# Kernel optimization log

Hardware: AMD Instinct MI355X
Metric: run time of the kernel (lower is better)

The kernel has to match this reference:

```python
import jax, jax.numpy as jnp
import numpy as np

NZ = 128
N_GEN = 8
BATCH = 2048
SLOPE = 0.2


def _convt(x, w, b, stride, pad):
    # PyTorch ConvTranspose2d(weight [Cin,Cout,kH,kW], stride, padding p)
    # == conv with lhs_dilation=stride, padding=k-1-p, spatially-flipped
    # kernel with in/out channels swapped.
    k = jnp.flip(w, axis=(2, 3)).transpose(2, 3, 0, 1)  # [kH,kW,Cin,Cout]
    y = jax.lax.conv_general_dilated(
        x, k, window_strides=(1, 1), padding=[(pad, pad), (pad, pad)],
        lhs_dilation=(stride, stride),
        dimension_numbers=('NCHW', 'HWIO', 'NCHW'))
    return y + b[None, :, None, None]


def setup_inputs() -> dict:
    key = jax.random.key(0)
    ks = jax.random.split(key, 12)
    s = 0.05
    return {
        'z': jax.random.normal(ks[0], (BATCH, NZ), jnp.float32),
        'g_idx': jax.random.randint(ks[1], (BATCH,), 0, N_GEN),
        'W1': jax.random.normal(ks[2], (N_GEN, NZ, 256), jnp.float32) * s,
        'b1': jax.random.normal(ks[3], (N_GEN, 256), jnp.float32) * s,
        'W2': jax.random.normal(ks[4], (N_GEN, 256, 1568), jnp.float32) * s,
        'b2': jax.random.normal(ks[5], (N_GEN, 1568), jnp.float32) * s,
        'cw1': jax.random.normal(ks[6], (N_GEN, 32, 16, 4, 4), jnp.float32) * s,
        'cb1': jax.random.normal(ks[7], (N_GEN, 16), jnp.float32) * s,
        'cw2': jax.random.normal(ks[8], (N_GEN, 16, 8, 4, 4), jnp.float32) * s,
        'cb2': jax.random.normal(ks[9], (N_GEN, 8), jnp.float32) * s,
        'cw3': jax.random.normal(ks[10], (N_GEN, 8, 1, 3, 3), jnp.float32) * s,
        'cb3': jax.random.normal(ks[11], (N_GEN, 1), jnp.float32) * s,
    }


def _single_gen(params, z):
    W1, b1, W2, b2, cw1, cb1, cw2, cb2, cw3, cb3 = params
    lrelu = lambda x: jax.nn.leaky_relu(x, SLOPE)
    h = lrelu(z @ W1 + b1)                 # [B,256]
    h = lrelu(h @ W2 + b2)                 # [B,1568]
    h = h.reshape(-1, 32, 7, 7)
    h = lrelu(_convt(h, cw1, cb1, 2, 2))   # [B,16,14,14]
    h = lrelu(_convt(h, cw2, cb2, 2, 2))   # [B,8,28,28]
    return jnp.tanh(_convt(h, cw3, cb3, 1, 1))  # [B,1,28,28]


def reference(z, g_idx, W1, b1, W2, b2, cw1, cb1, cw2, cb2, cw3, cb3):
    params = (W1, b1, W2, b2, cw1, cb1, cw2, cb2, cw3, cb3)
    # Compute every generator on the full batch (faithful to the torch loop),
    # vmapped over the generator axis: images [G,B,1,28,28].
    images = jax.vmap(_single_gen, in_axes=((0,) * 10, None))(params, z)
    # Per-sample gather: keep generator g_idx[b] for each sample b.
    return images[g_idx, jnp.arange(z.shape[0])]
```

## Files before the change

### kernel.cpp

```cpp
#include <hip/hip_runtime.h>
#include <cstdint>
#include <cstddef>

#define BATCH 2048
#define NZ 128
#define NGEN 8
#define GRPS 32
#define MAXG 72
#define NCT 13
#define H2_ELEMS 1792
#define WS_H1_OFF 16384
#define WS_H2_OFF (16384 + MAXG * 8192 * 4)
#define WS_W2T_OFF (WS_H2_OFF + BATCH * H2_ELEMS * 2)
#define W2T_GSTRIDE (1568 * 256)
#define NB_W2T (NGEN * 49)
#define NB_PREP (NB_W2T + MAXG * 4)
#define WS_WPK1_OFF (WS_W2T_OFF + NGEN * W2T_GSTRIDE * 2)
#define WS_WPK2_OFF (WS_WPK1_OFF + NGEN * 4096 * 4)
#define WS_WPK3_OFF (WS_WPK2_OFF + NGEN * 1024 * 4)
#define PS 168

typedef unsigned int u32;
typedef unsigned short u16;
typedef unsigned long long u64;
typedef _Float16 f16x8 __attribute__((ext_vector_type(8)));
typedef _Float16 f16x4 __attribute__((ext_vector_type(4)));
typedef _Float16 f16x2 __attribute__((ext_vector_type(2)));
typedef float f32x4 __attribute__((ext_vector_type(4)));

__device__ __forceinline__ float lrelu(float x) { return fmaxf(x, 0.2f * x); }
__device__ __forceinline__ u16 f16b(float f) {
    _Float16 h = (_Float16)f;
    return __builtin_bit_cast(u16, h);
}
__device__ __forceinline__ u32 pk2(float a, float b) {
    f16x2 v; v[0] = (_Float16)a; v[1] = (_Float16)b;
    return __builtin_bit_cast(u32, v);
}
__device__ __forceinline__ float dot2(u32 a, u32 b, float c) {
#if __has_builtin(__builtin_amdgcn_fdot2)
    return __builtin_amdgcn_fdot2(__builtin_bit_cast(f16x2, a),
                                  __builtin_bit_cast(f16x2, b), c, false);
#else
    float d;
    asm("v_dot2_f32_f16 %0, %1, %2, %3" : "=v"(d) : "v"(a), "v"(b), "v"(c));
    return d;
#endif
}
__device__ __forceinline__ float fast_tanh(float x) {
    x = fminf(fmaxf(x, -9.f), 9.f);
    const float e = __expf(2.f * x);
    return (e - 1.f) / (e + 1.f);
}
__device__ __forceinline__ int h2off(int n) {
    const int ci = n / 49, rm = n % 49;
    return ci * 56 + (rm / 7) * 8 + (rm % 7);
}

__global__ __launch_bounds__(256) void prep_kernel(
    const float* __restrict__ z, const int* __restrict__ g_idx,
    const float* __restrict__ W1, const float* __restrict__ b1,
    const float* __restrict__ W2, int* __restrict__ wsi,
    float* __restrict__ h1g, _Float16* __restrict__ W2T,
    const float* __restrict__ cw1, const float* __restrict__ cw2,
    const float* __restrict__ cw3,
    u32* __restrict__ wpk1, u32* __restrict__ wpk2, u32* __restrict__ wpk3)
{
    __shared__ __align__(16) char pmem[16896];

    const int tid = threadIdx.x;
    const int bx = blockIdx.x;

    if (bx < NB_W2T) {
        _Float16 (*t)[264] = (_Float16 (*)[264])pmem;
        const int g = bx / 49;
        const int n0 = (bx % 49) * 32;
        const float* src = W2 + (size_t)g * 256 * 1568;
        const int nl = tid & 31, kh = tid >> 5;
        #pragma unroll 8
        for (int p = 0; p < 32; ++p) {
            const int k = p * 8 + kh;
            t[nl][k] = (_Float16)src[(size_t)k * 1568 + n0 + nl];
        }
        __syncthreads();
        _Float16* dst = W2T + (size_t)g * W2T_GSTRIDE + (size_t)n0 * 256;
        #pragma unroll
        for (int ii = 0; ii < 4; ++ii) {
            const int i = tid + 256 * ii;
            const int n = i >> 5, kc = i & 31;
            *(uint4*)(dst + (size_t)n * 256 + kc * 8) = *(const uint4*)&t[n][kc * 8];
        }
        return;
    }

    if (bx >= NB_PREP && bx < NB_PREP + NGEN) {
        const int g = bx - NB_PREP;
        const float* c1p = cw1 + g * 8192;
        u32* o1 = wpk1 + g * 4096;
        for (int i = tid; i < 4096; i += 256) {
            const int cip = i >> 8, a = (i >> 6) & 3, co = (i >> 2) & 15, c = i & 3;
            const float* s = c1p + cip * 512 + co * 16 + a * 4 + c;
            o1[i] = pk2(s[0], s[256]);
        }
        const float* c2p = cw2 + g * 2048;
        u32* o2 = wpk2 + g * 1024;
        for (int i = tid; i < 1024; i += 256) {
            const int cip = i >> 7, a = (i >> 5) & 3, co = (i >> 2) & 7, c = i & 3;
            const float* s = c2p + cip * 256 + co * 16 + a * 4 + c;
            o2[i] = pk2(s[0], s[128]);
        }
        if (tid < 36) {
            const int cip = tid / 9, r = tid % 9;
            const float* s = cw3 + g * 72 + cip * 18 + r;
            wpk3[g * 36 + tid] = pk2(s[0], s[9]);
        }
        return;
    }

    u16* rank       = (u16*)pmem;
    int (*wcnt)[NGEN]  = (int (*)[NGEN])(pmem + 4096);
    int (*wboff)[NGEN] = (int (*)[NGEN])(pmem + 4224);
    int* pbase      = (int*)(pmem + 4352);
    const int w = tid >> 6, lane = tid & 63;
    if (tid < 4 * NGEN) wcnt[tid >> 3][tid & 7] = 0;
    __syncthreads();
    const u64 lt = ((u64)1 << lane) - 1;
    #pragma unroll
    for (int r = 0; r < 8; ++r) {
        const int b = r * 256 + tid;
        const int gg = g_idx[b];
        u64 m[NGEN];
        #pragma unroll
        for (int k = 0; k < NGEN; ++k) m[k] = __ballot(gg == k);
        rank[b] = (u16)((int)__popcll(m[gg] & lt) + wcnt[w][gg]);
        if (lane < NGEN) wcnt[w][lane] += (int)__popcll(m[lane]);
    }
    __syncthreads();
    if (tid == 0) {
        int acc = 0;
        for (int g = 0; g < NGEN; ++g) {
            pbase[g] = acc;
            const int tot = wcnt[0][g] + wcnt[1][g] + wcnt[2][g] + wcnt[3][g];
            acc += ((tot + GRPS - 1) / GRPS) * GRPS;
        }
        pbase[NGEN] = acc;
    }
    __syncthreads();
    if (tid < 32) {
        const int ww = tid >> 3, g = tid & 7;
        int off = pbase[g];
        for (int w2 = 0; w2 < ww; ++w2) off += wcnt[w2][g];
        wboff[ww][g] = off;
    }
    __syncthreads();

    if (bx >= NB_PREP + NGEN) {
        if (tid == 0) wsi[0] = pbase[NGEN];
        for (int i = tid; i < MAXG * GRPS; i += 256) wsi[16 + i] = -1;
        __syncthreads();
        #pragma unroll
        for (int r = 0; r < 8; ++r) {
            const int b = r * 256 + tid;
            const int gg = g_idx[b];
            wsi[16 + wboff[w][gg] + (int)rank[b]] = b;
        }
        return;
    }

    const int bx2 = bx - NB_W2T;
    const int grp = bx2 >> 2;
    const int s0 = (bx2 & 3) * 8;
    if (grp * GRPS >= pbase[NGEN]) return;

    int gsel = 0;
    #pragma unroll
    for (int g = 1; g < NGEN; ++g) if (grp * GRPS >= pbase[g]) gsel = g;

    int* sb = (int*)(pmem + 4400);
    float (*zst)[12] = (float (*)[12])(pmem + 4608);
    if (tid < 8) sb[tid] = -1;
    __syncthreads();
    const int base = grp * GRPS + s0;
    #pragma unroll
    for (int r = 0; r < 8; ++r) {
        const int b = r * 256 + tid;
        const int gg = g_idx[b];
        const int rel = wboff[w][gg] + (int)rank[b] - base;
        if ((unsigned)rel < 8u) sb[rel] = b;
    }
    __syncthreads();

    const float* W1g = W1 + gsel * (NZ * 256);
    const float* b1g = b1 + gsel * 256;

    {
        const int s = tid >> 5, f = tid & 31;
        float4 v = make_float4(0.f, 0.f, 0.f, 0.f);
        if (sb[s] >= 0) v = *(const float4*)(z + (size_t)sb[s] * NZ + 4 * f);
        zst[4 * f + 0][s] = v.x; zst[4 * f + 1][s] = v.y;
        zst[4 * f + 2][s] = v.z; zst[4 * f + 3][s] = v.w;
    }
    __syncthreads();

    const int c = tid;
    float acc[8];
    #pragma unroll
    for (int s = 0; s < 8; ++s) acc[s] = 0.f;
    const float* wp = W1g + c;
    #pragma unroll 4
    for (int k = 0; k < NZ; ++k) {
        const float wv = wp[k * 256];
        float av[8];
        *(float4*)&av[0] = *(const float4*)&zst[k][0];
        *(float4*)&av[4] = *(const float4*)&zst[k][4];
        #pragma unroll
        for (int s = 0; s < 8; ++s) acc[s] += av[s] * wv;
    }
    const float bv = b1g[c];
    float* hp = h1g + (size_t)grp * 8192 + (size_t)s0 * 256 + c;
    #pragma unroll
    for (int s = 0; s < 8; ++s) hp[s * 256] = lrelu(acc[s] + bv);
}

__global__ __launch_bounds__(256) void fc2_kernel(
    const int* __restrict__ g_idx,
    const _Float16* __restrict__ W2T, const float* __restrict__ b2,
    const int* __restrict__ wsi, const float* __restrict__ h1g,
    u16* __restrict__ h2g)
{
    __shared__ __align__(16) char afsm[16384];
    _Float16* afrag = (_Float16*)afsm;
    __shared__ int sb[GRPS];
    __shared__ int sG;

    const int tid = threadIdx.x;
    const int grp = blockIdx.x / NCT;
    const int tile = blockIdx.x % NCT;
    if (grp * GRPS >= wsi[0]) return;

    if (tid == 0) sG = g_idx[wsi[16 + grp * GRPS]];
    if (tid < GRPS) sb[tid] = wsi[16 + grp * GRPS + tid];
    __syncthreads();
    const _Float16* W2Tg = W2T + (size_t)sG * W2T_GSTRIDE;
    const float* b2g = b2 + sG * 1568;

    {
        const float4* h1p4 = (const float4*)(h1g + (size_t)grp * 8192);
        #pragma unroll
        for (int i = 0; i < 8; ++i) {
            const int u = tid + 256 * i;
            const int j4 = u & 1;
            const int ln = (u >> 1) & 63;
            const int kq = (u >> 7) & 7;
            const int mt = (u >> 10) & 1;
            const int s = mt * 16 + (ln & 15);
            const float4 v = h1p4[s * 64 + kq * 8 + ((ln >> 4) << 1) + j4];
            f16x4 hi;
            hi[0] = (_Float16)v.x; hi[1] = (_Float16)v.y;
            hi[2] = (_Float16)v.z; hi[3] = (_Float16)v.w;
            const int bh = ((mt * 8 + kq) * 64 + ln) * 8 + 4 * j4;
            *(f16x4*)&afrag[bh] = hi;
        }
    }
    __syncthreads();

    const int wave = tid >> 6;
    const int lane = tid & 63;
    const int q = lane >> 4;
    const int nl = lane & 15;
    const int nb0 = tile * 128 + 2 * wave * 16;
    const int nb1 = nb0 + 16;
    const bool act0 = nb0 < 1568, act1 = nb1 < 1568;

    f32x4 accA0 = {0.f, 0.f, 0.f, 0.f}, accB0 = accA0;
    f32x4 accA1 = accA0, accB1 = accA0;
    if (act0) {
        const _Float16* bp = W2Tg + (size_t)(nb0 + nl) * 256 + q * 8;
        #pragma unroll
        for (int kq = 0; kq < 8; ++kq) {
            const f16x8 b = *(const f16x8*)(bp + kq * 32);
            const f16x8 a0 = *(const f16x8*)&afrag[((0 * 8 + kq) * 64 + lane) * 8];
            const f16x8 a1 = *(const f16x8*)&afrag[((1 * 8 + kq) * 64 + lane) * 8];
            accA0 = __builtin_amdgcn_mfma_f32_16x16x32_f16(a0, b, accA0, 0, 0, 0);
            accB0 = __builtin_amdgcn_mfma_f32_16x16x32_f16(a1, b, accB0, 0, 0, 0);
        }
    }
    if (act1) {
        const _Float16* bp = W2Tg + (size_t)(nb1 + nl) * 256 + q * 8;
        #pragma unroll
        for (int kq = 0; kq < 8; ++kq) {
            const f16x8 b = *(const f16x8*)(bp + kq * 32);
            const f16x8 a0 = *(const f16x8*)&afrag[((0 * 8 + kq) * 64 + lane) * 8];
            const f16x8 a1 = *(const f16x8*)&afrag[((1 * 8 + kq) * 64 + lane) * 8];
            accA1 = __builtin_amdgcn_mfma_f32_16x16x32_f16(a0, b, accA1, 0, 0, 0);
            accB1 = __builtin_amdgcn_mfma_f32_16x16x32_f16(a1, b, accB1, 0, 0, 0);
        }
    }
    __syncthreads();

    u16* pst = (u16*)afsm;
    const int nstart = tile * 128;
    const int nend = (nstart + 128 < 1568) ? nstart + 128 : 1568;
    const int offLo = h2off(nstart), offHi = h2off(nend - 1);
    const int lo8 = offLo & ~7;

    if (act0) {
        const int n = nb0 + nl;
        const float bias = b2g[n];
        u16* pp = pst + (h2off(n) - lo8);
        #pragma unroll
        for (int reg = 0; reg < 4; ++reg) {
            pp[(q * 4 + reg) * PS]        = f16b(lrelu(accA0[reg] + bias));
            pp[(16 + q * 4 + reg) * PS]   = f16b(lrelu(accB0[reg] + bias));
        }
    }
    if (act1) {
        const int n = nb1 + nl;
        const float bias = b2g[n];
        u16* pp = pst + (h2off(n) - lo8);
        #pragma unroll
        for (int reg = 0; reg < 4; ++reg) {
            pp[(q * 4 + reg) * PS]        = f16b(lrelu(accA1[reg] + bias));
            pp[(16 + q * 4 + reg) * PS]   = f16b(lrelu(accB1[reg] + bias));
        }
    }
    __syncthreads();

    {
        const int s = tid >> 3, p = tid & 7;
        const int bb = sb[s];
        if (bb >= 0) {
            u16* row = h2g + (size_t)bb * H2_ELEMS;
            const u16* ps = pst + s * PS - lo8;
            const int c0 = (offLo + 7) & ~7;
            const int c1 = (offHi + 1) & ~7;
            for (int o = offLo + p; o < c0 && o <= offHi; o += 8) row[o] = ps[o];
            const int t0 = (c1 > offLo) ? c1 : offLo;
            for (int o = t0 + p; o <= offHi; o += 8) row[o] = ps[o];
            for (int c = c0 + p * 8; c + 8 <= c1; c += 64)
                *(uint4*)(row + c) = *(const uint4*)(ps + c);
        }
    }
}

template <int H>
__device__ __forceinline__ void conv2p_half(
    const u32 (*c1s)[14][20], u16* dst,
    const u32* __restrict__ w2g, const float bv, const int co, const int y)
{
    float acc[14];
    #pragma unroll
    for (int xx = 0; xx < 14; ++xx) acc[xx] = bv;
    const int a0 = (y + 1) & 1;
    for (int aa = 0; aa < 2; ++aa) {
        const int a = a0 + 2 * aa;
        const int iy = (y + 1 - a) >> 1;
        if ((unsigned)iy < 14u) {
            #pragma unroll 4
            for (int cip = 0; cip < 8; ++cip) {
                u32 rr[10];
                if (H == 0) {
                    *(uint4*)&rr[0] = *(const uint4*)&c1s[cip][iy][0];
                    *(uint4*)&rr[4] = *(const uint4*)&c1s[cip][iy][4];
                } else {
                    *(uint4*)&rr[0] = *(const uint4*)&c1s[cip][iy][4];
                    *(uint4*)&rr[4] = *(const uint4*)&c1s[cip][iy][8];
                    *(uint2*)&rr[8] = *(const uint2*)&c1s[cip][iy][12];
                }
                const uint4 wq = *(const uint4*)(w2g + ((cip * 4 + a) * 8 + co) * 4);
                const u32 wv[4] = {wq.x, wq.y, wq.z, wq.w};
                #pragma unroll
                for (int xx = 0; xx < 14; ++xx) {
                    const int x = 14 * H + xx;
                    const int c0v = (x + 1) & 1;
                    const int ix0 = (x + 1 - c0v) >> 1;
                    const int li = ix0 - 4 * H;
                    if (ix0 < 14) acc[xx] = dot2(rr[li],     wv[c0v],     acc[xx]);
                    if (ix0 >= 1) acc[xx] = dot2(rr[li - 1], wv[c0v + 2], acc[xx]);
                }
            }
        }
    }
    #pragma unroll
    for (int xx = 0; xx < 14; ++xx) dst[2 * (14 * H + xx)] = f16b(lrelu(acc[xx]));
}

__global__ __launch_bounds__(256, 6) void conv_kernel(
    const int* __restrict__ g_idx, const int* __restrict__ wsi,
    const u32* __restrict__ wpk1, const float* __restrict__ cb1,
    const u32* __restrict__ wpk2, const float* __restrict__ cb2,
    const u32* __restrict__ wpk3, const float* __restrict__ cb3,
    const u16* __restrict__ h2g, float* __restrict__ out)
{
    __shared__ __align__(16) char smem[8960 + 14784];
    u32 (*c1s)[14][20] = (u32 (*)[14][20])smem;
    u32 (*h2s)[7][8]   = (u32 (*)[7][8])(smem + 8960);
    u32 (*c2s)[28][33] = (u32 (*)[28][33])(smem + 8960);
    __shared__ u32 w3s[36];

    const int tid = threadIdx.x;
    const int b = wsi[16 + blockIdx.x];
    if (b < 0) return;
    const int g = g_idx[b];
    const u32* w1g = wpk1 + g * 4096;
    const u32* w2g = wpk2 + g * 1024;
    const float* cb1g = cb1 + g * 16;
    const float* cb2g = cb2 + g * 8;
    const float  cb3v = cb3[g];

    if (tid < 224) {
        const uint4 qv = ((const uint4*)(h2g + (size_t)b * H2_ELEMS))[tid];
        const int ci = tid / 7, yq = tid % 7;
        u16* dst = (u16*)&h2s[ci >> 1][yq][0] + (ci & 1);
        const u32 w[4] = {qv.x, qv.y, qv.z, qv.w};
        #pragma unroll
        for (int j = 0; j < 4; ++j) {
            dst[4 * j]     = (u16)(w[j] & 0xffffu);
            dst[4 * j + 2] = (u16)(w[j] >> 16);
        }
    }
    if (tid < 36) w3s[tid] = wpk3[g * 36 + tid];
    __syncthreads();

    if (tid < 224) {
        const int co = tid / 14, y = tid % 14;
        const float bv = cb1g[co];
        float acc[14];
        #pragma unroll
        for (int x = 0; x < 14; ++x) acc[x] = bv;
        const int a0 = (y + 1) & 1;
        for (int aa = 0; aa < 2; ++aa) {
            const int a = a0 + 2 * aa;
            const int iy = (y + 1 - a) >> 1;
            if ((unsigned)iy < 7u) {
                #pragma unroll 4
                for (int cip = 0; cip < 16; ++cip) {
                    u32 rr[8];
                    *(uint4*)&rr[0] = *(const uint4*)&h2s[cip][iy][0];
                    *(uint4*)&rr[4] = *(const uint4*)&h2s[cip][iy][4];
                    const uint4 wq = *(const uint4*)(w1g + ((cip * 4 + a) * 16 + co) * 4);
                    const u32 wv[4] = {wq.x, wq.y, wq.z, wq.w};
                    #pragma unroll
                    for (int x = 0; x < 14; ++x) {
                        const int c0v = (x + 1) & 1;
                        const int ix0 = (x + 1 - c0v) >> 1;
                        if (ix0 < 7)  acc[x] = dot2(rr[ix0],     wv[c0v],     acc[x]);
                        if (ix0 >= 1) acc[x] = dot2(rr[ix0 - 1], wv[c0v + 2], acc[x]);
                    }
                }
            }
        }
        u16* dst = (u16*)&c1s[co >> 1][y][0] + (co & 1);
        #pragma unroll
        for (int x = 0; x < 14; ++x) dst[2 * x] = f16b(lrelu(acc[x]));
    }
    __syncthreads();

    if (tid < 224) {
        const int co = tid / 28, y = tid % 28;
        const float bv = cb2g[co];
        u16* dst = (u16*)&c2s[co >> 1][y][0] + (co & 1);
        conv2p_half<0>(c1s, dst, w2g, bv, co, y);
        conv2p_half<1>(c1s, dst, w2g, bv, co, y);
    }
    __syncthreads();

    if (tid < 196) {
        const int y = tid / 7, qq = tid % 7;
        const int xb = qq * 4;
        float acc[4] = {cb3v, cb3v, cb3v, cb3v};
        #pragma unroll 2
        for (int cip = 0; cip < 4; ++cip) {
            u32 wp[9];
            #pragma unroll
            for (int j = 0; j < 9; ++j) wp[j] = w3s[cip * 9 + j];
            #pragma unroll
            for (int a = 0; a < 3; ++a) {
                const int iy = y + 1 - a;
                if ((unsigned)iy < 28u) {
                    u32 rr[6];
                    #pragma unroll
                    for (int j = 0; j < 6; ++j) {
                        const int ix = xb - 1 + j;
                        rr[j] = ((unsigned)ix < 28u) ? c2s[cip][iy][ix] : 0u;
                    }
                    #pragma unroll
                    for (int xx = 0; xx < 4; ++xx)
                        #pragma unroll
                        for (int c = 0; c < 3; ++c)
                            acc[xx] = dot2(rr[xx + 2 - c], wp[a * 3 + c], acc[xx]);
                }
            }
        }
        float* op = out + (size_t)b * 784 + y * 28 + xb;
        #pragma unroll
        for (int xx = 0; xx < 4; ++xx) op[xx] = fast_tanh(acc[xx]);
    }
}

extern "C" void kernel_launch(void* const* d_in, const int* in_sizes, int n_in,
                              void* d_out, int out_size, void* d_ws, size_t ws_size,
                              hipStream_t stream) {
    const float* z   = (const float*)d_in[0];
    const int*   gi  = (const int*)d_in[1];
    const float* W1  = (const float*)d_in[2];
    const float* b1  = (const float*)d_in[3];
    const float* W2  = (const float*)d_in[4];
    const float* b2  = (const float*)d_in[5];
    const float* cw1 = (const float*)d_in[6];
    const float* cb1 = (const float*)d_in[7];
    const float* cw2 = (const float*)d_in[8];
    const float* cb2 = (const float*)d_in[9];
    const float* cw3 = (const float*)d_in[10];
    const float* cb3 = (const float*)d_in[11];
    int*      wsi = (int*)d_ws;
    float*    h1g = (float*)((char*)d_ws + WS_H1_OFF);
    u16*      h2g = (u16*)((char*)d_ws + WS_H2_OFF);
    _Float16* w2t = (_Float16*)((char*)d_ws + WS_W2T_OFF);
    u32*      wpk1 = (u32*)((char*)d_ws + WS_WPK1_OFF);
    u32*      wpk2 = (u32*)((char*)d_ws + WS_WPK2_OFF);
    u32*      wpk3 = (u32*)((char*)d_ws + WS_WPK3_OFF);

    prep_kernel<<<NB_PREP + NGEN + 1, 256, 0, stream>>>(z, gi, W1, b1, W2, wsi,
                                                        h1g, w2t, cw1, cw2, cw3,
                                                        wpk1, wpk2, wpk3);
    fc2_kernel<<<MAXG * NCT, 256, 0, stream>>>(gi, w2t, b2, wsi, h1g, h2g);
    conv_kernel<<<MAXG * GRPS, 256, 0, stream>>>(gi, wsi, wpk1, cb1, wpk2, cb2,
                                                 wpk3, cb3, h2g, (float*)d_out);
}
```

Before: 163.9 us.

## Merge conv2 halves into one full-row pass and pad conv2 output for vector loads

Merges the two half-row passes of the second transposed conv into one 28-wide pass, so each c1 row and weight vector is read from LDS once instead of twice. The conv2 output buffer gets a zero border column on each side (stride 30 instead of 33), so the final 3x3 conv can use aligned uint2 LDS loads without bounds checks. Unroll factors drop from 4 to 2 to offset the larger 28-entry accumulator array. The extra registers may hurt occupancy under the 6-block launch bound, and the new stride can raise LDS bank conflicts.

```diff
diff --git a/kernel.cpp b/kernel.cpp
--- a/kernel.cpp
+++ b/kernel.cpp
@@ -343,46 +343,39 @@
     }
 }
 
-template <int H>
-__device__ __forceinline__ void conv2p_half(
+__device__ __forceinline__ void conv2p_full(
     const u32 (*c1s)[14][20], u16* dst,
     const u32* __restrict__ w2g, const float bv, const int co, const int y)
 {
-    float acc[14];
-    #pragma unroll
-    for (int xx = 0; xx < 14; ++xx) acc[xx] = bv;
+    float acc[28];
+    #pragma unroll
+    for (int x = 0; x < 28; ++x) acc[x] = bv;
     const int a0 = (y + 1) & 1;
     for (int aa = 0; aa < 2; ++aa) {
         const int a = a0 + 2 * aa;
         const int iy = (y + 1 - a) >> 1;
         if ((unsigned)iy < 14u) {
-            #pragma unroll 4
+            #pragma unroll 2
             for (int cip = 0; cip < 8; ++cip) {
-                u32 rr[10];
-                if (H == 0) {
-                    *(uint4*)&rr[0] = *(const uint4*)&c1s[cip][iy][0];
-                    *(uint4*)&rr[4] = *(const uint4*)&c1s[cip][iy][4];
-                } else {
-                    *(uint4*)&rr[0] = *(const uint4*)&c1s[cip][iy][4];
-                    *(uint4*)&rr[4] = *(const uint4*)&c1s[cip][iy][8];
-                    *(uint2*)&rr[8] = *(const uint2*)&c1s[cip][iy][12];
-                }
+                u32 rr[14];
+                *(uint4*)&rr[0]  = *(const uint4*)&c1s[cip][iy][0];
+                *(uint4*)&rr[4]  = *(const uint4*)&c1s[cip][iy][4];
+                *(uint4*)&rr[8]  = *(const uint4*)&c1s[cip][iy][8];
+                *(uint2*)&rr[12] = *(const uint2*)&c1s[cip][iy][12];
                 const uint4 wq = *(const uint4*)(w2g + ((cip * 4 + a) * 8 + co) * 4);
                 const u32 wv[4] = {wq.x, wq.y, wq.z, wq.w};
                 #pragma unroll
-                for (int xx = 0; xx < 14; ++xx) {
-                    const int x = 14 * H + xx;
+                for (int x = 0; x < 28; ++x) {
                     const int c0v = (x + 1) & 1;
                     const int ix0 = (x + 1 - c0v) >> 1;
-                    const int li = ix0 - 4 * H;
-                    if (ix0 < 14) acc[xx] = dot2(rr[li],     wv[c0v],     acc[xx]);
-                    if (ix0 >= 1) acc[xx] = dot2(rr[li - 1], wv[c0v + 2], acc[xx]);
+                    if (ix0 < 14) acc[x] = dot2(rr[ix0],     wv[c0v],     acc[x]);
+                    if (ix0 >= 1) acc[x] = dot2(rr[ix0 - 1], wv[c0v + 2], acc[x]);
                 }
             }
         }
     }
     #pragma unroll
-    for (int xx = 0; xx < 14; ++xx) dst[2 * (14 * H + xx)] = f16b(lrelu(acc[xx]));
+    for (int x = 0; x < 28; ++x) dst[2 * (1 + x)] = f16b(lrelu(acc[x]));
 }
 
 __global__ __launch_bounds__(256, 6) void conv_kernel(
@@ -392,10 +385,10 @@
     const u32* __restrict__ wpk3, const float* __restrict__ cb3,
     const u16* __restrict__ h2g, float* __restrict__ out)
 {
-    __shared__ __align__(16) char smem[8960 + 14784];
+    __shared__ __align__(16) char smem[8960 + 13440];
     u32 (*c1s)[14][20] = (u32 (*)[14][20])smem;
     u32 (*h2s)[7][8]   = (u32 (*)[7][8])(smem + 8960);
-    u32 (*c2s)[28][33] = (u32 (*)[28][33])(smem + 8960);
+    u32 (*c2s)[28][30] = (u32 (*)[28][30])(smem + 8960);
     __shared__ u32 w3s[36];
 
     const int tid = threadIdx.x;
@@ -433,7 +426,7 @@
             const int a = a0 + 2 * aa;
             const int iy = (y + 1 - a) >> 1;
             if ((unsigned)iy < 7u) {
-                #pragma unroll 4
+                #pragma unroll 2
                 for (int cip = 0; cip < 16; ++cip) {
                     u32 rr[8];
                     *(uint4*)&rr[0] = *(const uint4*)&h2s[cip][iy][0];
@@ -457,11 +450,12 @@
     __syncthreads();
 
     if (tid < 224) {
+        const int zc = tid / 56, zr = tid % 56;
+        c2s[zc][zr % 28][(zr < 28) ? 0 : 29] = 0u;
         const int co = tid / 28, y = tid % 28;
         const float bv = cb2g[co];
         u16* dst = (u16*)&c2s[co >> 1][y][0] + (co & 1);
-        conv2p_half<0>(c1s, dst, w2g, bv, co, y);
-        conv2p_half<1>(c1s, dst, w2g, bv, co, y);
+        conv2p_full(c1s, dst, w2g, bv, co, y);
     }
     __syncthreads();
 
@@ -479,11 +473,9 @@
                 const int iy = y + 1 - a;
                 if ((unsigned)iy < 28u) {
                     u32 rr[6];
-                    #pragma unroll
-                    for (int j = 0; j < 6; ++j) {
-                        const int ix = xb - 1 + j;
-                        rr[j] = ((unsigned)ix < 28u) ? c2s[cip][iy][ix] : 0u;
-                    }
+                    *(uint2*)&rr[0] = *(const uint2*)&c2s[cip][iy][xb];
+                    *(uint2*)&rr[2] = *(const uint2*)&c2s[cip][iy][xb + 2];
+                    *(uint2*)&rr[4] = *(const uint2*)&c2s[cip][iy][xb + 4];
                     #pragma unroll
                     for (int xx = 0; xx < 4; ++xx)
                         #pragma unroll
```

Measured after the change: 162.5 us. Within noise of the previous version (-0.9%).
